# Optimization experiments

Hardware: AMD Instinct MI355X
Metric: run time of the kernel (lower is better)

Reference implementation:

```python
import jax, jax.numpy as jnp
import numpy as np

V, D, L, T, B, H = 32000, 1024, 3, 1024, 4, 8
Dh = D // H
NC = 2
LAT = 24
FRACTAL_DIM = 1.5  # fixed inside original forward


def _nrm(x):
    return jnp.linalg.norm(x, axis=-1, keepdims=True)


def _ln(x, w, b):
    m = x.mean(-1, keepdims=True)
    v = ((x - m) ** 2).mean(-1, keepdims=True)
    return (x - m) / jnp.sqrt(v + 1e-5) * w + b


def _forward(input_ids, tok_table, emb_scales, emb_norm, pos_emb, W_el, b_el,
             W_le, b_le, ecs, epres, ln1_w, ln1_b, ln2_w, ln2_b,
             qW, qb, kW, kb, vW, vb, oW, ob, f1W, f1b, f2W, f2b,
             alpha, fscale, enorm, clsW, clsb):
    # --- GenuineEmbedding ---
    tok = tok_table[input_ids]                      # [B,T,D]
    enh = tok * emb_scales
    enh = enh * (_nrm(tok) / (_nrm(enh) + 1e-8)) * emb_norm
    x = enh + pos_emb[None, :, :]
    # --- Leech lattice encode ---
    ie = _nrm(x)
    proj = x @ W_el + b_el                          # [B,T,24]
    lp = jnp.round(proj / ecs) * ecs
    enc = lp * (ie / (_nrm(lp) + 1e-8)) * epres
    # --- Leech lattice decode ---
    ie2 = _nrm(enc)
    corr = jnp.where(jnp.abs(enc) > ecs, enc, jnp.zeros_like(enc))
    dec = corr @ W_le + b_le                        # [B,T,D]
    dec = dec * (ie2 / (_nrm(dec) + 1e-8)) * epres
    x = x + dec
    # spectral filter frequencies (shared across layers)
    freqs = jnp.fft.fftfreq(T)
    kmag = jnp.clip(jnp.abs(freqs), 1e-10, None)
    log_atan = jnp.arctan(jnp.log(kmag))            # [T]
    scale = 1.0 / np.sqrt(Dh)
    for i in range(L):
        # --- spectral attention ---
        h = _ln(x, ln1_w[i], ln1_b[i])
        aa = alpha[i] + fscale[i] * (FRACTAL_DIM - 1.5)
        filt = jnp.exp(-aa * log_atan)[None, :, None, None]  # [1,T,1,1]
        q = (h @ qW[i] + qb[i]).reshape(B, T, H, Dh)
        k = (h @ kW[i] + kb[i]).reshape(B, T, H, Dh)
        v = (h @ vW[i] + vb[i]).reshape(B, T, H, Dh)
        qf = (jnp.fft.fft(q, axis=1) * filt).real
        kf = (jnp.fft.fft(k, axis=1) * filt).real
        vf = (jnp.fft.fft(v, axis=1) * filt).real
        logits = jnp.einsum('bthd,bshd->bhts', qf, kf) * scale
        w = jax.nn.softmax(logits, axis=-1)
        att = jnp.einsum('bhts,bshd->bthd', w, vf).reshape(B, T, D)
        out = att @ oW[i] + ob[i]
        out = out * (_nrm(h) / (_nrm(out) + 1e-8)) * enorm[i]
        x = x + out  # dropout inactive (eval)
        # --- FFN ---
        h2 = _ln(x, ln2_w[i], ln2_b[i])
        y = jax.nn.gelu(h2 @ f1W[i] + f1b[i], approximate=False) @ f2W[i] + f2b[i]
        x = x + y
    pooled = x.mean(axis=1)                         # [B,D]
    return pooled @ clsW + clsb                     # [B,NC]


def setup_inputs() -> dict:
    key = jax.random.key(0)
    ks = jax.random.split(key, 16)
    def n(k, shape):
        return jax.random.normal(k, shape, jnp.float32) * 0.02
    return {
        'input_ids': jax.random.randint(ks[0], (B, T), 0, V),
        'tok_table': jax.random.normal(ks[1], (V, D), jnp.float32),
        'emb_scales': jnp.ones((D,), jnp.float32),
        'emb_norm': jnp.float32(1.0),
        'pos_emb': jax.random.normal(ks[2], (T, D), jnp.float32),
        'W_el': n(ks[3], (D, LAT)), 'b_el': jnp.zeros((LAT,), jnp.float32),
        'W_le': n(ks[4], (LAT, D)), 'b_le': jnp.zeros((D,), jnp.float32),
        'ecs': jnp.float32(0.1), 'epres': jnp.float32(1.0),
        'ln1_w': jnp.ones((L, D), jnp.float32), 'ln1_b': jnp.zeros((L, D), jnp.float32),
        'ln2_w': jnp.ones((L, D), jnp.float32), 'ln2_b': jnp.zeros((L, D), jnp.float32),
        'qW': n(ks[5], (L, D, D)), 'qb': jnp.zeros((L, D), jnp.float32),
        'kW': n(ks[6], (L, D, D)), 'kb': jnp.zeros((L, D), jnp.float32),
        'vW': n(ks[7], (L, D, D)), 'vb': jnp.zeros((L, D), jnp.float32),
        'oW': n(ks[8], (L, D, D)), 'ob': jnp.zeros((L, D), jnp.float32),
        'f1W': n(ks[9], (L, D, 4 * D)), 'f1b': jnp.zeros((L, 4 * D), jnp.float32),
        'f2W': n(ks[10], (L, 4 * D, D)), 'f2b': jnp.zeros((L, D), jnp.float32),
        'alpha': jnp.full((L,), 1.5, jnp.float32),
        'fscale': jnp.full((L,), 0.5, jnp.float32),
        'enorm': jnp.ones((L,), jnp.float32),
        'clsW': n(ks[11], (D, NC)), 'clsb': jnp.zeros((NC,), jnp.float32),
    }


def reference(input_ids, tok_table, emb_scales, emb_norm, pos_emb, W_el, b_el,
              W_le, b_le, ecs, epres, ln1_w, ln1_b, ln2_w, ln2_b,
              qW, qb, kW, kb, vW, vb, oW, ob, f1W, f1b, f2W, f2b,
              alpha, fscale, enorm, clsW, clsb):
    return _forward(input_ids, tok_table, emb_scales, emb_norm, pos_emb, W_el, b_el,
                    W_le, b_le, ecs, epres, ln1_w, ln1_b, ln2_w, ln2_b,
                    qW, qb, kW, kb, vW, vb, oW, ob, f1W, f1b, f2W, f2b,
                    alpha, fscale, enorm, clsW, clsb)
```

## Files before the change

kernel.cpp:

```cpp
#include <hip/hip_runtime.h>
#include <math.h>

#define TS    1024
#define DM    1024
#define BB    4
#define HH    8
#define LL    3
#define NLAT  24
#define NROWS 4096
#define DFF   4096

typedef _Float16 f16x8 __attribute__((ext_vector_type(8)));
typedef float f32x4 __attribute__((ext_vector_type(4)));
typedef unsigned short u16x4 __attribute__((ext_vector_type(4)));
typedef unsigned short u16x8 __attribute__((ext_vector_type(8)));

__device__ __forceinline__ unsigned short f16h(float x) {
  _Float16 h = (_Float16)x;
  return __builtin_bit_cast(unsigned short, h);
}
__device__ __forceinline__ float f16tof(unsigned short u) {
  _Float16 h = __builtin_bit_cast(_Float16, u);
  return (float)h;
}
__device__ __forceinline__ void gl16(const void* g, void* l) {
  __builtin_amdgcn_global_load_lds(
      (const __attribute__((address_space(1))) void*)g,
      (__attribute__((address_space(3))) void*)l, 16, 0, 0);
}

template <int N>
__device__ __forceinline__ void wait_vm() {
  static_assert(N == 0 || N == 2 || N == 3 || N == 4 || N == 5 || N == 6 ||
                N == 8 || N == 10 || N == 12 || N == 16, "vmcnt literal");
  if constexpr (N == 0) asm volatile("s_waitcnt vmcnt(0)" ::: "memory");
  else if constexpr (N == 2) asm volatile("s_waitcnt vmcnt(2)" ::: "memory");
  else if constexpr (N == 3) asm volatile("s_waitcnt vmcnt(3)" ::: "memory");
  else if constexpr (N == 4) asm volatile("s_waitcnt vmcnt(4)" ::: "memory");
  else if constexpr (N == 5) asm volatile("s_waitcnt vmcnt(5)" ::: "memory");
  else if constexpr (N == 6) asm volatile("s_waitcnt vmcnt(6)" ::: "memory");
  else if constexpr (N == 8) asm volatile("s_waitcnt vmcnt(8)" ::: "memory");
  else if constexpr (N == 10) asm volatile("s_waitcnt vmcnt(10)" ::: "memory");
  else if constexpr (N == 12) asm volatile("s_waitcnt vmcnt(12)" ::: "memory");
  else asm volatile("s_waitcnt vmcnt(16)" ::: "memory");
}

__device__ __forceinline__ float waveAllSum(float v) {
#pragma unroll
  for (int m = 32; m >= 1; m >>= 1) v += __shfl_xor(v, m);
  return v;
}
__device__ __forceinline__ float waveAllMax(float v) {
#pragma unroll
  for (int m = 32; m >= 1; m >>= 1) v = fmaxf(v, __shfl_xor(v, m));
  return v;
}
__device__ __forceinline__ float blockSum(float v, float* red, int nw) {
  v = waveAllSum(v);
  int lane = threadIdx.x & 63, wid = threadIdx.x >> 6;
  __syncthreads();
  if (lane == 0) red[wid] = v;
  __syncthreads();
  float t = 0.f;
  for (int i = 0; i < nw; i++) t += red[i];
  return t;
}
__device__ __forceinline__ float blockMax(float v, float* red, int nw) {
  v = waveAllMax(v);
  int lane = threadIdx.x & 63, wid = threadIdx.x >> 6;
  __syncthreads();
  if (lane == 0) red[wid] = v;
  __syncthreads();
  float t = -INFINITY;
  for (int i = 0; i < nw; i++) t = fmaxf(t, red[i]);
  return t;
}

__global__ __launch_bounds__(256) void build_C_pp(unsigned short* __restrict__ ch,
                                                  unsigned short* __restrict__ cl) {
  int i = blockIdx.x * 256 + threadIdx.x;
  int t = i >> 10, s = i & 1023;
  int m = (t * s) & 1023;
  float ang = (float)m * 6.135923151542565e-3f;
  float c = cosf(ang);
  unsigned short h = f16h(c);
  ch[i] = h;
  cl[i] = f16h(c - f16tof(h));
}

__global__ void build_filt(float* __restrict__ filt,
                           const float* __restrict__ alpha,
                           const float* __restrict__ fscale) {
  int t = threadIdx.x;
  float fr = (t < 512) ? (float)t : (float)(t - 1024);
  fr *= (1.0f / 1024.0f);
  float km = fmaxf(fabsf(fr), 1e-10f);
  float la = atanf(logf(km));
  for (int l = 0; l < LL; l++) {
    float aa = alpha[l] + fscale[l] * (1.5f - 1.5f);
    filt[l * TS + t] = expf(-aa * la);
  }
}

__global__ void biascat3(const float* __restrict__ qb, const float* __restrict__ kb,
                         const float* __restrict__ vb, float* __restrict__ out) {
  int i = blockIdx.x * 256 + threadIdx.x;
  const float* s = (i < 1024) ? qb : ((i < 2048) ? kb : vb);
  out[i] = s[i & 1023];
}

__global__ __launch_bounds__(256) void trans_wel(const float* __restrict__ W_el,
                                                 float* __restrict__ W_elT) {
  int i = blockIdx.x * 256 + threadIdx.x;
  int j = i >> 10, d = i & 1023;
  W_elT[i] = W_el[(size_t)d * NLAT + j];
}

__global__ __launch_bounds__(256) void embed_kernel(
    const int* __restrict__ ids, const float* __restrict__ tok_table,
    const float* __restrict__ emb_scales, const float* __restrict__ emb_norm,
    const float* __restrict__ pos_emb, float* __restrict__ x) {
  __shared__ float red[4];
  int row = blockIdx.x;
  int t = row & (TS - 1);
  int tid = threadIdx.x;
  const float* tok = tok_table + (size_t)ids[row] * DM;
  float ev[4];
  float st = 0.f, se = 0.f;
#pragma unroll
  for (int kk = 0; kk < 4; kk++) {
    int d = tid + kk * 256;
    float tv = tok[d];
    float e = tv * emb_scales[d];
    ev[kk] = e;
    st += tv * tv;
    se += e * e;
  }
  st = blockSum(st, red, 4);
  se = blockSum(se, red, 4);
  float sc = sqrtf(st) / (sqrtf(se) + 1e-8f) * emb_norm[0];
  float* xr = x + (size_t)row * DM;
  const float* pr = pos_emb + (size_t)t * DM;
#pragma unroll
  for (int kk = 0; kk < 4; kk++) {
    int d = tid + kk * 256;
    xr[d] = ev[kk] * sc + pr[d];
  }
}

__global__ __launch_bounds__(256) void leech_wave(
    float* __restrict__ x, const float* __restrict__ W_elT,
    const float* __restrict__ b_el, const float* __restrict__ W_le,
    const float* __restrict__ b_le, const float* __restrict__ ecs_p,
    const float* __restrict__ epres_p) {
  int tid = threadIdx.x;
  int wv = tid >> 6, lane = tid & 63;
  int row = blockIdx.x * 4 + wv;
  float ecs = ecs_p[0], epres = epres_p[0];
  float* xr = x + (size_t)row * DM;

  float acc[NLAT];
#pragma unroll
  for (int j = 0; j < NLAT; j++) acc[j] = 0.f;
  float sx = 0.f;
  for (int kk = 0; kk < 16; kk++) {
    int d = lane + 64 * kk;
    float v = xr[d];
    sx += v * v;
#pragma unroll
    for (int j = 0; j < NLAT; j++) acc[j] = fmaf(v, W_elT[j * DM + d], acc[j]);
  }
  sx = waveAllSum(sx);
  float ie = sqrtf(sx);
#pragma unroll
  for (int j = 0; j < NLAT; j++) acc[j] = waveAllSum(acc[j]);

  float corr[NLAT];
  float slp = 0.f;
#pragma unroll
  for (int j = 0; j < NLAT; j++) {
    float l = rintf((acc[j] + b_el[j]) / ecs) * ecs;
    acc[j] = l;
    slp = fmaf(l, l, slp);
  }
  float nlp = sqrtf(slp);
  float s1 = ie / (nlp + 1e-8f) * epres;
  float ie2 = fabsf(s1) * nlp;
#pragma unroll
  for (int j = 0; j < NLAT; j++) {
    float e = acc[j] * s1;
    corr[j] = (fabsf(e) > ecs) ? e : 0.f;
  }

  float sd = 0.f;
  for (int kk = 0; kk < 16; kk++) {
    int d = lane + 64 * kk;
    float v = b_le[d];
#pragma unroll
    for (int j = 0; j < NLAT; j++) v = fmaf(corr[j], W_le[j * DM + d], v);
    sd = fmaf(v, v, sd);
  }
  sd = waveAllSum(sd);
  float sc2 = ie2 / (sqrtf(sd) + 1e-8f) * epres;

  for (int kk = 0; kk < 16; kk++) {
    int d = lane + 64 * kk;
    float v = b_le[d];
#pragma unroll
    for (int j = 0; j < NLAT; j++) v = fmaf(corr[j], W_le[j * DM + d], v);
    xr[d] = fmaf(v, sc2, xr[d]);
  }
}

__global__ __launch_bounds__(256) void ln_pp(
    const float* __restrict__ x, const float* __restrict__ w,
    const float* __restrict__ b, unsigned short* __restrict__ oHi,
    unsigned short* __restrict__ oLo, float* __restrict__ hnorm) {
  __shared__ float red[4];
  int row = blockIdx.x, tid = threadIdx.x;
  const float4 v = ((const float4*)(x + (size_t)row * DM))[tid];
  float s = v.x + v.y + v.z + v.w;
  s = blockSum(s, red, 4);
  float mean = s * (1.f / 1024.f);
  float dx = v.x - mean, dy = v.y - mean, dz = v.z - mean, dw = v.w - mean;
  float ss = dx * dx + dy * dy + dz * dz + dw * dw;
  ss = blockSum(ss, red, 4);
  float inv = 1.f / sqrtf(ss * (1.f / 1024.f) + 1e-5f);
  const float4 wv = ((const float4*)w)[tid];
  const float4 bv = ((const float4*)b)[tid];
  float hv[4];
  hv[0] = dx * inv * wv.x + bv.x;
  hv[1] = dy * inv * wv.y + bv.y;
  hv[2] = dz * inv * wv.z + bv.z;
  hv[3] = dw * inv * wv.w + bv.w;
  u16x4 hh;
#pragma unroll
  for (int j = 0; j < 4; j++) hh[j] = f16h(hv[j]);
  *(u16x4*)(oHi + (size_t)row * DM + tid * 4) = hh;
  if (oLo) {
    u16x4 ll;
#pragma unroll
    for (int j = 0; j < 4; j++) ll[j] = f16h(hv[j] - f16tof(hh[j]));
    *(u16x4*)(oLo + (size_t)row * DM + tid * 4) = ll;
  }
  if (hnorm) {
    float hs = hv[0]*hv[0] + hv[1]*hv[1] + hv[2]*hv[2] + hv[3]*hv[3];
    hs = blockSum(hs, red, 4);
    if (tid == 0) hnorm[row] = sqrtf(hs);
  }
}

__global__ __launch_bounds__(256) void tsplit_f32(
    const float* __restrict__ in, unsigned short* __restrict__ oHi,
    unsigned short* __restrict__ oLo, int ldin, int ldout, float scale) {
  __shared__ float T[64][65];
  int r0 = blockIdx.y * 64, c0 = blockIdx.x * 64;
  int tid = threadIdx.x;
  int r = tid >> 2, s = tid & 3;
  const float* ip = in + (size_t)(r0 + r) * ldin + c0 + s * 16;
#pragma unroll
  for (int q = 0; q < 4; q++) {
    float4 v = ((const float4*)ip)[q];
    T[r][s * 16 + q * 4 + 0] = v.x;
    T[r][s * 16 + q * 4 + 1] = v.y;
    T[r][s * 16 + q * 4 + 2] = v.z;
    T[r][s * 16 + q * 4 + 3] = v.w;
  }
  __syncthreads();
  u16x8 h0, h1, l0, l1;
#pragma unroll
  for (int q = 0; q < 16; q++) {
    float v = T[s * 16 + q][r] * scale;
    unsigned short h = f16h(v);
    if (q < 8) h0[q] = h; else h1[q - 8] = h;
    if (oLo) {
      unsigned short l = f16h(v - f16tof(h));
      if (q < 8) l0[q] = l; else l1[q - 8] = l;
    }
  }
  size_t ob = (size_t)(c0 + r) * ldout + r0 + s * 16;
  *(u16x8*)(oHi + ob) = h0;
  *(u16x8*)(oHi + ob + 8) = h1;
  if (oLo) {
    *(u16x8*)(oLo + ob) = l0;
    *(u16x8*)(oLo + ob + 8) = l1;
  }
}

__global__ __launch_bounds__(256) void tsplit_u16(
    const unsigned short* __restrict__ in, unsigned short* __restrict__ out,
    int ldin, int ldout, long sIn, long sOut) {
  __shared__ unsigned short T[64][68];
  int z = blockIdx.z;
  in += (size_t)z * sIn;
  out += (size_t)z * sOut;
  int r0 = blockIdx.y * 64, c0 = blockIdx.x * 64;
  int tid = threadIdx.x;
  int r = tid >> 2, s = tid & 3;
  const unsigned short* ip = in + (size_t)(r0 + r) * ldin + c0 + s * 16;
  u16x8 a = *(const u16x8*)ip;
  u16x8 b = *(const u16x8*)(ip + 8);
#pragma unroll
  for (int q = 0; q < 8; q++) {
    T[r][s * 16 + q] = a[q];
    T[r][s * 16 + 8 + q] = b[q];
  }
  __syncthreads();
  u16x8 o0, o1;
#pragma unroll
  for (int q = 0; q < 8; q++) {
    o0[q] = T[s * 16 + q][r];
    o1[q] = T[s * 16 + 8 + q][r];
  }
  size_t ob = (size_t)(c0 + r) * ldout + r0 + s * 16;
  *(u16x8*)(out + ob) = o0;
  *(u16x8*)(out + ob + 8) = o1;
}

enum { E_PP = 0, E_QKV, E_F32, E_F32_BIAS, E_P1_GELU, E_F32_ACC_BIAS, E_F32_ATOMIC, E_V };

template <int EPI, bool ALO, bool BLO, int TMI, int DEPTH, int NKC = 4>
__global__ __launch_bounds__(256, 2) void gemmT(
    const unsigned short* __restrict__ Ah, const unsigned short* __restrict__ Al,
    const unsigned short* __restrict__ Bh, const unsigned short* __restrict__ Bl,
    void* __restrict__ C, void* __restrict__ C2, void* __restrict__ C3,
    void* __restrict__ C4, void* __restrict__ C5,
    const float* __restrict__ bias, const float* __restrict__ filtp, float desc,
    int K, int lda, int ldb, int ldc, int zdiv,
    long sAa, long sAb, long sBa, long sBb, long sCa, long sCb) {
  constexpr int NMA = 1 + (ALO ? 1 : 0);
  constexpr int NMB = 1 + (BLO ? 1 : 0);
  constexpr int HA = TMI / 64;
  constexpr int CA = NMA * NKC * HA;
  constexpr int CB = NMB * NKC * 2;
  constexpr int CPW = (CA + CB) / 4;
  constexpr int MI = TMI / 32;
  constexpr int BK = NKC * 8;
  constexpr int NBUF = DEPTH + 1;
  __shared__ __align__(16) unsigned short smA[NBUF][NMA][NKC][TMI][8];
  __shared__ __align__(16) unsigned short smB[NBUF][NMB][NKC][128][8];

  const int gx = gridDim.x, gy = gridDim.y;
  const int nb = gx * gy * gridDim.z;
  const int lid = (blockIdx.z * gy + blockIdx.y) * gx + blockIdx.x;
  const int cpx = nb >> 3;
  const int swz = (lid & 7) * cpx + (lid >> 3);
  const int bxi = swz % gx;
  const int tmp2 = swz / gx;
  const int byi = tmp2 % gy;
  const int bzi = tmp2 / gy;

  const int w = threadIdx.x >> 6, lane = threadIdx.x & 63;
  const int wm = w >> 1, wn = w & 1;
  const int bm = byi * TMI, bn = bxi * 128;
  const int za = bzi / zdiv, zb = bzi % zdiv;
  const long Ao = (long)za * sAa + (long)zb * sAb;
  const long Bo = (long)za * sBa + (long)zb * sBb;

  f32x4 acc[MI][4];
#pragma unroll
  for (int i = 0; i < MI; i++)
#pragma unroll
    for (int j = 0; j < 4; j++) acc[i][j] = (f32x4){0.f, 0.f, 0.f, 0.f};

  auto stage = [&](int buf, int k0) {
#pragma unroll
    for (int c = 0; c < CPW; c++) {
      int id = w + 4 * c;
      if (id < CA) {
        int pl = id / (NKC * HA);
        int rem = id - pl * NKC * HA;
        int kc = rem / HA, half = rem - kc * HA;
        const unsigned short* src =
            (pl ? Al : Ah) + Ao + (size_t)(bm + half * 64 + lane) * lda + k0 + kc * 8;
        gl16(src, (void*)&smA[buf][pl][kc][half * 64][0]);
      } else {
        int bid = id - CA;
        int pl = bid / (NKC * 2);
        int rem = bid - pl * NKC * 2;
        int kc = rem >> 1, half = rem & 1;
        const unsigned short* src =
            (pl ? Bl : Bh) + Bo + (size_t)(bn + half * 64 + lane) * ldb + k0 + kc * 8;
        gl16(src, (void*)&smB[buf][pl][kc][half * 64][0]);
      }
    }
  };

  const int nt = K / BK;
  stage(0, 0);
  if (DEPTH == 2 && nt > 1) stage(1, BK);
  int cur = 0, nxt = (DEPTH == 2) ? 2 : 1;
  for (int t = 0; t < nt; t++) {
    if constexpr (DEPTH == 1) {
      if (t + 1 < nt) {
        stage(nxt, (t + 1) * BK);
        wait_vm<CPW>();
      } else {
        wait_vm<0>();
      }
    } else {
      if (t + 2 < nt) {
        stage(nxt, (t + 2) * BK);
        wait_vm<2 * CPW>();
      } else if (t + 1 < nt) {
        wait_vm<CPW>();
      } else {
        wait_vm<0>();
      }
    }
    __builtin_amdgcn_s_barrier();
    __builtin_amdgcn_sched_barrier(0);

    const int fr = lane & 15, kc2 = lane >> 4;
#pragma unroll
    for (int kb = 0; kb < NKC / 4; kb++) {
      const int kcc = 4 * kb + kc2;
      f16x8 ah[MI], bh[4], alx[MI], blx[4];
#pragma unroll
      for (int i = 0; i < MI; i++) {
        ah[i] = *(const f16x8*)&smA[cur][0][kcc][wm * (TMI / 2) + i * 16 + fr][0];
        if (ALO) alx[i] = *(const f16x8*)&smA[cur][NMA - 1][kcc][wm * (TMI / 2) + i * 16 + fr][0];
      }
#pragma unroll
      for (int j = 0; j < 4; j++) {
        bh[j] = *(const f16x8*)&smB[cur][0][kcc][wn * 64 + j * 16 + fr][0];
        if (BLO) blx[j] = *(const f16x8*)&smB[cur][NMB - 1][kcc][wn * 64 + j * 16 + fr][0];
      }
#pragma unroll
      for (int i = 0; i < MI; i++)
#pragma unroll
        for (int j = 0; j < 4; j++) {
          acc[i][j] = __builtin_amdgcn_mfma_f32_16x16x32_f16(ah[i], bh[j], acc[i][j], 0, 0, 0);
          if (BLO) acc[i][j] = __builtin_amdgcn_mfma_f32_16x16x32_f16(ah[i], blx[j], acc[i][j], 0, 0, 0);
          if (ALO) acc[i][j] = __builtin_amdgcn_mfma_f32_16x16x32_f16(alx[i], bh[j], acc[i][j], 0, 0, 0);
        }
    }
    __builtin_amdgcn_sched_barrier(0);
    __builtin_amdgcn_s_barrier();
    cur = (cur == NBUF - 1) ? 0 : cur + 1;
    nxt = (nxt == NBUF - 1) ? 0 : nxt + 1;
  }

  const int fr0 = lane & 15, rg = lane >> 4;
  const int colb = bn + wn * 64 + fr0;
  const int rowb = bm + wm * (TMI / 2) + rg * 4;
  const long Co = (long)za * sCa + (long)zb * sCb;
#pragma unroll
  for (int i = 0; i < MI; i++)
#pragma unroll
    for (int j = 0; j < 4; j++)
#pragma unroll
      for (int r = 0; r < 4; r++) {
        int row = rowb + i * 16 + r;
        int col = colb + j * 16;
        float v = acc[i][j][r] * desc;
        long idx = Co + (long)row * ldc + col;
        if constexpr (EPI == E_PP) {
          unsigned short h = f16h(v);
          ((unsigned short*)C)[idx] = h;
          ((unsigned short*)C2)[idx] = f16h(v - f16tof(h));
        } else if constexpr (EPI == E_QKV) {
          int t2 = row & (TS - 1);
          v *= filtp[t2];
          if (t2 == 0) v = fmaf(1024.f * filtp[0], bias[col], v);
          int seg = col >> 10, nn = col & 1023;
          long oix = (long)row * 1024 + nn;
          if (seg == 0) {
            unsigned short h = f16h(v);
            ((unsigned short*)C)[oix] = h;
            ((unsigned short*)C2)[oix] = f16h(v - f16tof(h));
          } else {
            unsigned short h = f16h(v);
            ((unsigned short*)C3)[oix] = h;
            ((unsigned short*)C4)[oix] = f16h(v - f16tof(h));
          }
        } else if constexpr (EPI == E_V) {
          int t2 = row & (TS - 1);
          v *= filtp[t2];
          if (t2 == 0) v = fmaf(1024.f * filtp[0], bias[col], v);
          ((unsigned short*)C)[idx] = f16h(v);
        } else if constexpr (EPI == E_F32) {
          ((float*)C)[idx] = v;
        } else if constexpr (EPI == E_F32_BIAS) {
          ((float*)C)[idx] = v + bias[col];
        } else if constexpr (EPI == E_P1_GELU) {
          v += bias[col];
          v = 0.5f * v * (1.f + erff(v * 0.7071067811865476f));
          ((unsigned short*)C)[idx] = f16h(v);
        } else if constexpr (EPI == E_F32_ACC_BIAS) {
          ((float*)C)[idx] += v + bias[col];
        } else {
          if (za == 0) v += bias[col];
          atomicAdd(&((float*)C)[(long)row * ldc + col], v);
        }
      }
}

__global__ __launch_bounds__(256) void softmax_p(const float* __restrict__ S,
                                                 unsigned short* __restrict__ P,
                                                 float scale) {
  __shared__ float red[4];
  int row = blockIdx.x, tid = threadIdx.x;
  float4 v = ((const float4*)(S + (size_t)row * 1024))[tid];
  v.x *= scale; v.y *= scale; v.z *= scale; v.w *= scale;
  float m = fmaxf(fmaxf(v.x, v.y), fmaxf(v.z, v.w));
  m = blockMax(m, red, 4);
  float4 e;
  e.x = expf(v.x - m); e.y = expf(v.y - m); e.z = expf(v.z - m); e.w = expf(v.w - m);
  float s = e.x + e.y + e.z + e.w;
  s = blockSum(s, red, 4);
  float inv = 1.f / s;
  u16x4 o;
  o[0] = f16h(e.x * inv); o[1] = f16h(e.y * inv);
  o[2] = f16h(e.z * inv); o[3] = f16h(e.w * inv);
  *(u16x4*)(P + (size_t)row * 1024 + tid * 4) = o;
}

__global__ __launch_bounds__(256) void outscale_kernel(
    float* __restrict__ x, const float* __restrict__ outp,
    const float* __restrict__ hnorm, const float* __restrict__ enorm_l) {
  __shared__ float red[4];
  int row = blockIdx.x, tid = threadIdx.x;
  float4 v = ((const float4*)(outp + (size_t)row * DM))[tid];
  float ss = v.x * v.x + v.y * v.y + v.z * v.z + v.w * v.w;
  ss = blockSum(ss, red, 4);
  float sc = hnorm[row] / (sqrtf(ss) + 1e-8f) * enorm_l[0];
  float4* xp = (float4*)(x + (size_t)row * DM);
  float4 xv = xp[tid];
  xv.x = fmaf(v.x, sc, xv.x);
  xv.y = fmaf(v.y, sc, xv.y);
  xv.z = fmaf(v.z, sc, xv.z);
  xv.w = fmaf(v.w, sc, xv.w);
  xp[tid] = xv;
}

__global__ __launch_bounds__(256) void pool_partial(const float* __restrict__ x,
                                                    float* __restrict__ part) {
  int b = blockIdx.x, c = blockIdx.y, tid = threadIdx.x;
  const float* xb = x + ((size_t)b * TS + c * 64) * DM;
  float4 s = {0.f, 0.f, 0.f, 0.f};
  for (int r = 0; r < 64; r++) {
    float4 v = ((const float4*)(xb + (size_t)r * DM))[tid];
    s.x += v.x; s.y += v.y; s.z += v.z; s.w += v.w;
  }
  ((float4*)(part + (size_t)(b * 16 + c) * DM))[tid] = s;
}
__global__ __launch_bounds__(1024) void pool_cls2(const float* __restrict__ part,
                                                  const float* __restrict__ clsW,
                                                  const float* __restrict__ clsb,
                                                  float* __restrict__ out) {
  __shared__ float red[16];
  int b = blockIdx.x, d = threadIdx.x;
  float s = 0.f;
  for (int c = 0; c < 16; c++) s += part[(size_t)(b * 16 + c) * DM + d];
  float p = s * (1.f / 1024.f);
  float a0 = p * clsW[d * 2 + 0];
  float a1 = p * clsW[d * 2 + 1];
  a0 = blockSum(a0, red, 16);
  a1 = blockSum(a1, red, 16);
  if (d == 0) {
    out[b * 2 + 0] = a0 + clsb[0];
    out[b * 2 + 1] = a1 + clsb[1];
  }
}

extern "C" void kernel_launch(void* const* d_in, const int* in_sizes, int n_in,
                              void* d_out, int out_size, void* d_ws, size_t ws_size,
                              hipStream_t stream) {
  (void)in_sizes; (void)n_in; (void)out_size; (void)ws_size;
  const int*   ids        = (const int*)  d_in[0];
  const float* tok_table  = (const float*)d_in[1];
  const float* emb_scales = (const float*)d_in[2];
  const float* emb_norm   = (const float*)d_in[3];
  const float* pos_emb    = (const float*)d_in[4];
  const float* W_el       = (const float*)d_in[5];
  const float* b_el       = (const float*)d_in[6];
  const float* W_le       = (const float*)d_in[7];
  const float* b_le       = (const float*)d_in[8];
  const float* ecs        = (const float*)d_in[9];
  const float* epres      = (const float*)d_in[10];
  const float* ln1_w      = (const float*)d_in[11];
  const float* ln1_b      = (const float*)d_in[12];
  const float* ln2_w      = (const float*)d_in[13];
  const float* ln2_b      = (const float*)d_in[14];
  const float* qW = (const float*)d_in[15]; const float* qb = (const float*)d_in[16];
  const float* kW = (const float*)d_in[17]; const float* kb = (const float*)d_in[18];
  const float* vW = (const float*)d_in[19]; const float* vb = (const float*)d_in[20];
  const float* oW = (const float*)d_in[21]; const float* ob = (const float*)d_in[22];
  const float* f1W = (const float*)d_in[23]; const float* f1b = (const float*)d_in[24];
  const float* f2W = (const float*)d_in[25]; const float* f2b = (const float*)d_in[26];
  const float* alpha  = (const float*)d_in[27];
  const float* fscale = (const float*)d_in[28];
  const float* enorm  = (const float*)d_in[29];
  const float* clsW   = (const float*)d_in[30];
  const float* clsb   = (const float*)d_in[31];

  const size_t MB = 1u << 20;
  const long M1 = 1048576;
  char* p = (char*)d_ws;
  auto take = [&](size_t n) { char* r = p; p += n; return r; };
  unsigned short* CtH = (unsigned short*)take(2 * MB);
  unsigned short* CtL = (unsigned short*)take(2 * MB);
  float* filt    = (float*)take(16 * 1024);
  float* hnorm   = (float*)take(16 * 1024);
  float* bias3   = (float*)take(16 * 1024);
  float* W_elT   = (float*)take(128 * 1024);
  float* part    = (float*)take(1 * MB);
  float* x       = (float*)take(16 * MB);
  unsigned short* BIG = (unsigned short*)take(64 * MB);
  unsigned short* Hh  = BIG,            *Hl  = BIG + 4 * M1;
  unsigned short* HTh = BIG + 8 * M1,   *HTl = BIG + 12 * M1;
  unsigned short* HCh = BIG + 16 * M1,  *HCl = BIG + 20 * M1;
  unsigned short* WTh = BIG + 24 * M1,  *WTl = BIG + 28 * M1;
  unsigned short* P   = BIG;
  unsigned short* QFh = (unsigned short*)take(8 * MB);
  unsigned short* QFl = (unsigned short*)take(8 * MB);
  unsigned short* KFh = (unsigned short*)take(8 * MB);
  unsigned short* KFl = (unsigned short*)take(8 * MB);
  unsigned short* VT  = (unsigned short*)take(8 * MB);
  float* SREG = (float*)take(32 * MB);
  unsigned short* atth = (unsigned short*)SREG;
  unsigned short* attl = atth + 4 * M1;
  float* OUTP = SREG + 4 * M1;
  unsigned short* MID = (unsigned short*)SREG;
  unsigned short* Vtmp = HTh;

  const float WS = 1024.f;
  const float DS = 1.f / 1024.f;
  const float scale = 0.08838834764831845f;

  build_C_pp<<<4096, 256, 0, stream>>>(CtH, CtL);
  build_filt<<<1, 1024, 0, stream>>>(filt, alpha, fscale);
  trans_wel<<<96, 256, 0, stream>>>(W_el, W_elT);
  embed_kernel<<<NROWS, 256, 0, stream>>>(ids, tok_table, emb_scales, emb_norm, pos_emb, x);
  leech_wave<<<1024, 256, 0, stream>>>(x, W_elT, b_el, W_le, b_le, ecs, epres);

  dim3 t44(16, 16, 4), t11(16, 16, 1);
  for (int i = 0; i < LL; i++) {
    ln_pp<<<NROWS, 256, 0, stream>>>(x, ln1_w + i * DM, ln1_b + i * DM, Hh, Hl, hnorm);
    tsplit_u16<<<dim3(16, 16, 8), 256, 0, stream>>>(Hh, HTh, 1024, 1024, M1, M1);
    gemmT<E_PP, true, true, 64, 2><<<dim3(8, 16, 4), 256, 0, stream>>>(
        CtH, CtL, HTh, HTl, HCh, HCl, nullptr, nullptr, nullptr,
        nullptr, nullptr, 1.f, 1024, 1024, 1024, 1024, 1, 0, 0, M1, 0, M1, 0);
    tsplit_f32<<<t11, 256, 0, stream>>>(qW + (size_t)i * M1, WTh, WTl, 1024, 1024, WS);
    tsplit_f32<<<t11, 256, 0, stream>>>(kW + (size_t)i * M1, WTh + M1, WTl + M1, 1024, 1024, WS);
    tsplit_f32<<<t11, 256, 0, stream>>>(vW + (size_t)i * M1, WTh + 2 * M1, nullptr, 1024, 1024, WS);
    biascat3<<<12, 256, 0, stream>>>(qb + i * DM, kb + i * DM, vb + i * DM, bias3);
    gemmT<E_QKV, true, true, 128, 1><<<dim3(16, 32, 1), 256, 0, stream>>>(
        HCh, HCl, WTh, WTl, QFh, QFl, KFh, KFl, nullptr,
        bias3, filt + i * TS, DS, 1024, 1024, 1024, 1024, 1, 0, 0, 0, 0, 0, 0);
    gemmT<E_V, false, false, 64, 2><<<dim3(8, 64, 1), 256, 0, stream>>>(
        HCh, nullptr, WTh + 2 * M1, nullptr, Vtmp, nullptr, nullptr, nullptr, nullptr,
        vb + i * DM, filt + i * TS, DS, 1024, 1024, 1024, 1024, 1, 0, 0, 0, 0, 0, 0);
    tsplit_u16<<<t44, 256, 0, stream>>>(Vtmp, VT, 1024, 1024, M1, M1);
    for (int b = 0; b < BB; b++) {
      gemmT<E_F32, true, true, 128, 1><<<dim3(8, 8, 8), 256, 0, stream>>>(
          QFh + (size_t)b * M1, QFl + (size_t)b * M1,
          KFh + (size_t)b * M1, KFl + (size_t)b * M1,
          SREG, nullptr, nullptr, nullptr, nullptr,
          nullptr, nullptr, 1.f, 128, 1024, 1024, 1024, 1, 128, 0, 128, 0, M1, 0);
      softmax_p<<<HH * TS, 256, 0, stream>>>(SREG, P + (size_t)b * 8 * M1, scale);
    }
    gemmT<E_PP, false, false, 64, 2><<<dim3(1, 16, 32), 256, 0, stream>>>(
        P, nullptr, VT, nullptr, atth, attl, nullptr, nullptr, nullptr,
        nullptr, nullptr, 1.f, 1024, 1024, 1024, 1024, 8,
        8L * M1, M1, M1, 131072, M1, 128);
    hipMemsetAsync(OUTP, 0, 16 * MB, stream);
    tsplit_f32<<<t11, 256, 0, stream>>>(oW + (size_t)i * M1, WTh, nullptr, 1024, 1024, WS);
    gemmT<E_F32_ATOMIC, false, false, 128, 1><<<dim3(8, 32, 2), 256, 0, stream>>>(
        atth, nullptr, WTh, nullptr, OUTP, nullptr, nullptr, nullptr, nullptr,
        ob + i * DM, nullptr, DS, 512, 1024, 1024, 1024, 1, 512, 0, 512, 0, 0, 0);
    outscale_kernel<<<NROWS, 256, 0, stream>>>(x, OUTP, hnorm, enorm + i);
    ln_pp<<<NROWS, 256, 0, stream>>>(x, ln2_w + i * DM, ln2_b + i * DM, Hh, nullptr, nullptr);
    tsplit_f32<<<dim3(64, 16, 1), 256, 0, stream>>>(f1W + (size_t)i * 4 * M1, WTh, nullptr, 4096, 1024, WS);
    gemmT<E_P1_GELU, false, false, 128, 1, 8><<<dim3(32, 32, 1), 256, 0, stream>>>(
        Hh, nullptr, WTh, nullptr, MID, nullptr, nullptr, nullptr, nullptr,
        f1b + i * DFF, nullptr, DS, 1024, 1024, 1024, 4096, 1, 0, 0, 0, 0, 0, 0);
    tsplit_f32<<<dim3(16, 64, 1), 256, 0, stream>>>(f2W + (size_t)i * 4 * M1, WTh, nullptr, 1024, 4096, WS);
    gemmT<E_F32_ATOMIC, false, false, 128, 1, 8><<<dim3(8, 32, 2), 256, 0, stream>>>(
        MID, nullptr, WTh, nullptr, x, nullptr, nullptr, nullptr, nullptr,
        f2b + i * DM, nullptr, DS, 2048, 4096, 4096, 1024, 1, 2048, 0, 2048, 0, 0, 0);
  }
  pool_partial<<<dim3(BB, 16), 256, 0, stream>>>(x, part);
  pool_cls2<<<BB, 1024, 0, stream>>>(part, clsW, clsb, (float*)d_out);
}
```

Measured before the change: 1.906 ms.

## Add 128x256-tile 512-thread fp16 MFMA GEMM for feed-forward layers

Measured after the change: 1.934 ms. Within noise of the previous version (+1.5%).

```diff
diff --git a/kernel.cpp b/kernel.cpp
--- a/kernel.cpp
+++ b/kernel.cpp
@@ -496,6 +496,109 @@
       }
 }
 
+template <int EPI>
+__global__ __launch_bounds__(512, 4) void gemmW(
+    const unsigned short* __restrict__ A, const unsigned short* __restrict__ B,
+    void* __restrict__ C, const float* __restrict__ bias, float desc,
+    int K, int lda, int ldb, int ldc, long sAa, long sBa) {
+  __shared__ __align__(16) unsigned short smA[2][4][128][8];
+  __shared__ __align__(16) unsigned short smB[2][4][256][8];
+
+  const int gx = gridDim.x, gy = gridDim.y;
+  const int nb = gx * gy * gridDim.z;
+  const int lid = (blockIdx.z * gy + blockIdx.y) * gx + blockIdx.x;
+  const int cpx = nb >> 3;
+  const int swz = (lid & 7) * cpx + (lid >> 3);
+  const int bxi = swz % gx;
+  const int tmp2 = swz / gx;
+  const int byi = tmp2 % gy;
+  const int za  = tmp2 / gy;
+
+  const int w = threadIdx.x >> 6, lane = threadIdx.x & 63;
+  const int wm = w >> 2, wn = w & 3;
+  const int bm = byi * 128, bn = bxi * 256;
+  const long Ao = (long)za * sAa;
+  const long Bo = (long)za * sBa;
+
+  f32x4 acc[4][4];
+#pragma unroll
+  for (int i = 0; i < 4; i++)
+#pragma unroll
+    for (int j = 0; j < 4; j++) acc[i][j] = (f32x4){0.f, 0.f, 0.f, 0.f};
+
+  auto stage = [&](int buf, int k0) {
+#pragma unroll
+    for (int c = 0; c < 3; c++) {
+      int id = w + 8 * c;
+      if (id < 8) {
+        int kc = id >> 1, half = id & 1;
+        const unsigned short* src =
+            A + Ao + (size_t)(bm + half * 64 + lane) * lda + k0 + kc * 8;
+        gl16(src, (void*)&smA[buf][kc][half * 64][0]);
+      } else {
+        int bid = id - 8;
+        int kc = bid >> 2, q = bid & 3;
+        const unsigned short* src =
+            B + Bo + (size_t)(bn + q * 64 + lane) * ldb + k0 + kc * 8;
+        gl16(src, (void*)&smB[buf][kc][q * 64][0]);
+      }
+    }
+  };
+
+  const int nt = K >> 5;
+  stage(0, 0);
+  int cur = 0;
+  for (int t = 0; t < nt; t++) {
+    if (t + 1 < nt) {
+      stage(cur ^ 1, (t + 1) * 32);
+      wait_vm<3>();
+    } else {
+      wait_vm<0>();
+    }
+    __builtin_amdgcn_s_barrier();
+    __builtin_amdgcn_sched_barrier(0);
+
+    const int fr = lane & 15, kc2 = lane >> 4;
+    f16x8 ah[4], bh[4];
+#pragma unroll
+    for (int i = 0; i < 4; i++)
+      ah[i] = *(const f16x8*)&smA[cur][kc2][wm * 64 + i * 16 + fr][0];
+#pragma unroll
+    for (int j = 0; j < 4; j++)
+      bh[j] = *(const f16x8*)&smB[cur][kc2][wn * 64 + j * 16 + fr][0];
+#pragma unroll
+    for (int i = 0; i < 4; i++)
+#pragma unroll
+      for (int j = 0; j < 4; j++)
+        acc[i][j] = __builtin_amdgcn_mfma_f32_16x16x32_f16(ah[i], bh[j], acc[i][j], 0, 0, 0);
+    __builtin_amdgcn_sched_barrier(0);
+    __builtin_amdgcn_s_barrier();
+    cur ^= 1;
+  }
+
+  const int fr0 = lane & 15, rg = lane >> 4;
+  const int colb = bn + wn * 64 + fr0;
+  const int rowb = bm + wm * 64 + rg * 4;
+#pragma unroll
+  for (int i = 0; i < 4; i++)
+#pragma unroll
+    for (int j = 0; j < 4; j++)
+#pragma unroll
+      for (int r = 0; r < 4; r++) {
+        int row = rowb + i * 16 + r;
+        int col = colb + j * 16;
+        float v = acc[i][j][r] * desc;
+        if constexpr (EPI == E_P1_GELU) {
+          v += bias[col];
+          v = 0.5f * v * (1.f + erff(v * 0.7071067811865476f));
+          ((unsigned short*)C)[(long)row * ldc + col] = f16h(v);
+        } else {
+          if (za == 0) v += bias[col];
+          atomicAdd(&((float*)C)[(long)row * ldc + col], v);
+        }
+      }
+}
+
 __global__ __launch_bounds__(256) void softmax_p(const float* __restrict__ S,
                                                  unsigned short* __restrict__ P,
                                                  float scale) {
@@ -673,13 +776,11 @@
     outscale_kernel<<<NROWS, 256, 0, stream>>>(x, OUTP, hnorm, enorm + i);
     ln_pp<<<NROWS, 256, 0, stream>>>(x, ln2_w + i * DM, ln2_b + i * DM, Hh, nullptr, nullptr);
     tsplit_f32<<<dim3(64, 16, 1), 256, 0, stream>>>(f1W + (size_t)i * 4 * M1, WTh, nullptr, 4096, 1024, WS);
-    gemmT<E_P1_GELU, false, false, 128, 1, 8><<<dim3(32, 32, 1), 256, 0, stream>>>(
-        Hh, nullptr, WTh, nullptr, MID, nullptr, nullptr, nullptr, nullptr,
-        f1b + i * DFF, nullptr, DS, 1024, 1024, 1024, 4096, 1, 0, 0, 0, 0, 0, 0);
+    gemmW<E_P1_GELU><<<dim3(16, 32, 1), 512, 0, stream>>>(
+        Hh, WTh, MID, f1b + i * DFF, DS, 1024, 1024, 1024, 4096, 0, 0);
     tsplit_f32<<<dim3(16, 64, 1), 256, 0, stream>>>(f2W + (size_t)i * 4 * M1, WTh, nullptr, 1024, 4096, WS);
-    gemmT<E_F32_ATOMIC, false, false, 128, 1, 8><<<dim3(8, 32, 2), 256, 0, stream>>>(
-        MID, nullptr, WTh, nullptr, x, nullptr, nullptr, nullptr, nullptr,
-        f2b + i * DM, nullptr, DS, 2048, 4096, 4096, 1024, 1, 2048, 0, 2048, 0, 0, 0);
+    gemmW<E_F32_ATOMIC><<<dim3(4, 32, 4), 512, 0, stream>>>(
+        MID, WTh, x, f2b + i * DM, DS, 1024, 4096, 4096, 1024, 1024, 1024);
   }
   pool_partial<<<dim3(BB, 16), 256, 0, stream>>>(x, part);
   pool_cls2<<<BB, 1024, 0, stream>>>(part, clsW, clsb, (float*)d_out);
```
